# Optimization experiments

Hardware: AMD Instinct MI355X
Metric: run time of the kernel (lower is better)

## Reference

```python
import jax, jax.numpy as jnp
import numpy as np

D_MODEL = 384
D_STATE = 16
D_CONV = 3
EXPAND = 2
D_INNER = EXPAND * D_MODEL          # 768
DT_RANK = (D_MODEL + 15) // 16      # 24 (mamba_ssm 'auto' rank = ceil(d_model/16))
B_, H_, W_ = 8, 32, 32


def setup_inputs() -> dict:
    key = jax.random.key(0)
    ks = jax.random.split(key, 8)
    s = lambda k, shape, scale: jax.random.normal(k, shape, jnp.float32) * scale
    x = jax.random.normal(ks[0], (B_, D_MODEL, H_, W_), jnp.float32)
    in_proj_w = s(ks[1], (2 * D_INNER, D_MODEL), 0.02)
    conv_w = s(ks[2], (D_INNER, D_CONV), 0.1)          # depthwise conv kernels
    conv_b = jnp.zeros((D_INNER,), jnp.float32)
    x_proj_w = s(ks[3], (DT_RANK + 2 * D_STATE, D_INNER), 0.02)
    dt_proj_w = s(ks[4], (D_INNER, DT_RANK), 0.1)
    # bias so that softplus(bias) ~= 0.01 (mamba dt init)
    dt_proj_b = jnp.log(jnp.expm1(jnp.full((D_INNER,), 0.01, jnp.float32)))
    # S4D-real init: A = -[1..N] per channel, stored as log
    A_log = jnp.log(jnp.broadcast_to(
        jnp.arange(1, D_STATE + 1, dtype=jnp.float32), (D_INNER, D_STATE)))
    D = jnp.ones((D_INNER,), jnp.float32)
    out_proj_w = s(ks[5], (D_MODEL, D_INNER), 0.02)
    return dict(x=x, in_proj_w=in_proj_w, conv_w=conv_w, conv_b=conv_b,
                x_proj_w=x_proj_w, dt_proj_w=dt_proj_w, dt_proj_b=dt_proj_b,
                A_log=A_log, D=D, out_proj_w=out_proj_w)


def _mamba(xseq, in_proj_w, conv_w, conv_b, x_proj_w,
           dt_proj_w, dt_proj_b, A_log, D, out_proj_w):
    # xseq: (B, L, d_model)
    B, L, _ = xseq.shape
    xz = xseq @ in_proj_w.T                         # (B, L, 2*d_inner)
    xin, z = jnp.split(xz, 2, axis=-1)

    # depthwise causal conv1d over L
    xc = jnp.transpose(xin, (0, 2, 1))              # (B, d_inner, L)
    xc = jnp.pad(xc, ((0, 0), (0, 0), (D_CONV - 1, 0)))
    xc = jax.lax.conv_general_dilated(
        xc, conv_w[:, None, :], (1,), 'VALID',
        dimension_numbers=('NCH', 'OIH', 'NCH'),
        feature_group_count=D_INNER)
    xc = xc + conv_b[None, :, None]
    u = jax.nn.silu(jnp.transpose(xc, (0, 2, 1)))   # (B, L, d_inner)

    dbc = u @ x_proj_w.T                            # (B, L, dt_rank + 2N)
    dt = dbc[..., :DT_RANK]
    Bm = dbc[..., DT_RANK:DT_RANK + D_STATE]        # (B, L, N)
    Cm = dbc[..., DT_RANK + D_STATE:]               # (B, L, N)
    dt = jax.nn.softplus(dt @ dt_proj_w.T + dt_proj_b)  # (B, L, d_inner)
    A = -jnp.exp(A_log)                             # (d_inner, N)

    def step(h, inp):
        dt_t, B_t, C_t, u_t = inp                   # (B,d), (B,N), (B,N), (B,d)
        dA = jnp.exp(dt_t[..., None] * A)           # (B, d_inner, N)
        h = dA * h + (dt_t * u_t)[..., None] * B_t[:, None, :]
        y = jnp.einsum('bdn,bn->bd', h, C_t)
        return h, y

    h0 = jnp.zeros((B, D_INNER, D_STATE), xseq.dtype)
    _, ys = jax.lax.scan(step, h0, (jnp.swapaxes(dt, 0, 1), jnp.swapaxes(Bm, 0, 1),
                                    jnp.swapaxes(Cm, 0, 1), jnp.swapaxes(u, 0, 1)))
    y = jnp.swapaxes(ys, 0, 1) + u * D              # (B, L, d_inner)
    y = y * jax.nn.silu(z)
    return y @ out_proj_w.T                         # (B, L, d_model)


def reference(x, in_proj_w, conv_w, conv_b, x_proj_w,
              dt_proj_w, dt_proj_b, A_log, D, out_proj_w):
    # x: (B, C, H, W) -> sequence (B, H*W, C) -> Mamba -> back to (B, C, H, W)
    B, C, H, W = x.shape
    xseq = jnp.transpose(x, (0, 2, 3, 1)).reshape(B, H * W, C)
    y = _mamba(xseq, in_proj_w, conv_w, conv_b, x_proj_w,
               dt_proj_w, dt_proj_b, A_log, D, out_proj_w)
    return jnp.transpose(y.reshape(B, H, W, C), (0, 3, 1, 2))
```

## Files before the change

### kernel.cpp

```cpp
#include <hip/hip_runtime.h>

#define D_MODEL 384
#define D_STATE 16
#define D_INNER 768
#define DT_RANK 24
#define NB 8
#define LSEQ 1024
#define NROWS (NB * LSEQ)
#define DBC_N 56
#define SEG 16
#define NSEG 64

typedef unsigned short u16;
typedef __attribute__((ext_vector_type(8))) short bf16x8;
typedef __attribute__((ext_vector_type(4))) float f32x4;

__device__ __forceinline__ float silu(float x) { return x / (1.f + __expf(-x)); }

__device__ __forceinline__ u16 f2bf_rne(float v, float& hval) {
    unsigned u = __builtin_bit_cast(unsigned, v);
    unsigned h = (u + 0x7FFFu + ((u >> 16) & 1u)) >> 16;
    hval = __builtin_bit_cast(float, h << 16);
    return (u16)h;
}

__device__ __forceinline__ void split2(float v, u16& h, u16& l) {
    float hval, dummy;
    h = f2bf_rne(v, hval);
    l = f2bf_rne(v - hval, dummy);
}

template <int CTRL>
__device__ __forceinline__ float dpp_mov(float v) {
    return __builtin_bit_cast(float, __builtin_amdgcn_update_dpp(
        0, __builtin_bit_cast(int, v), CTRL, 0xf, 0xf, false));
}

__global__ __launch_bounds__(256) void k_splits(const float* __restrict__ Wi,
                                                const float* __restrict__ Wo,
                                                const float* __restrict__ Wx,
                                                u16* __restrict__ Wi_hi, u16* __restrict__ Wi_lo,
                                                u16* __restrict__ Wo_hi, u16* __restrict__ Wo_lo,
                                                u16* __restrict__ Wx_hi, u16* __restrict__ Wx_lo) {
    const int NWi = 1536 * 384, NWo = 384 * 768, NWx = 64 * 768;
    const int i = blockIdx.x * 256 + threadIdx.x;
    if (i < NWi) {
        u16 h, l; split2(Wi[i], h, l);
        Wi_hi[i] = h; Wi_lo[i] = l;
    } else if (i < NWi + NWo) {
        const int j = i - NWi;
        u16 h, l; split2(Wo[j], h, l);
        Wo_hi[j] = h; Wo_lo[j] = l;
    } else if (i < NWi + NWo + NWx) {
        const int j = i - NWi - NWo;
        const int row = j / 768;
        u16 h = 0, l = 0;
        if (row < DBC_N) split2(Wx[j], h, l);
        Wx_hi[j] = h; Wx_lo[j] = l;
    }
}

__global__ __launch_bounds__(256) void k_splitT(const float* __restrict__ src,
                                                u16* __restrict__ hi, u16* __restrict__ lo,
                                                int R) {
    __shared__ float s[32][33];
    const int r0 = blockIdx.x * 32, c0 = blockIdx.y * 32, b = blockIdx.z;
    const int t = threadIdx.x;
    const int cc = t & 31, rr = t >> 5;
#pragma unroll
    for (int p = 0; p < 4; ++p)
        s[rr + p * 8][cc] = src[((size_t)b * R + r0 + rr + p * 8) * LSEQ + c0 + cc];
    __syncthreads();
    const int rr2 = t & 31, cc2 = t >> 5;
#pragma unroll
    for (int p = 0; p < 4; ++p) {
        const int c = cc2 + p * 8;
        u16 h, l;
        split2(s[rr2][c], h, l);
        const size_t idx = ((size_t)b * LSEQ + c0 + c) * R + r0 + rr2;
        hi[idx] = h; lo[idx] = l;
    }
}

template <int K>
__global__ __launch_bounds__(256) void k_gemm(const u16* __restrict__ Ahi,
                                              const u16* __restrict__ Alo,
                                              const u16* __restrict__ Bhi,
                                              const u16* __restrict__ Blo,
                                              float* __restrict__ out0,
                                              float* __restrict__ out1) {
    constexpr int KT = K / 32;
    __shared__ u16 lA[2][2][512 * 8];
    __shared__ u16 lB[2][2][512 * 8];
    const int tid = threadIdx.x;
    const int n0 = blockIdx.x * 128;
    const int m0 = blockIdx.y * 128;

    bf16x8 rah[2], ral[2], rbh[2], rbl[2];
    auto load_kt = [&](int kt) {
        const int ko = kt * 32;
#pragma unroll
        for (int i = 0; i < 2; ++i) {
            const int slot = tid + 256 * i;
            const size_t aoff = (size_t)(m0 + (slot & 127)) * K + ko + (slot >> 7) * 8;
            const size_t boff = (size_t)(n0 + (slot & 127)) * K + ko + (slot >> 7) * 8;
            rah[i] = *reinterpret_cast<const bf16x8*>(Ahi + aoff);
            ral[i] = *reinterpret_cast<const bf16x8*>(Alo + aoff);
            rbh[i] = *reinterpret_cast<const bf16x8*>(Bhi + boff);
            rbl[i] = *reinterpret_cast<const bf16x8*>(Blo + boff);
        }
    };
    auto write_kt = [&](int buf) {
#pragma unroll
        for (int i = 0; i < 2; ++i) {
            const int slot = tid + 256 * i;
            *reinterpret_cast<bf16x8*>(&lA[buf][0][slot * 8]) = rah[i];
            *reinterpret_cast<bf16x8*>(&lA[buf][1][slot * 8]) = ral[i];
            *reinterpret_cast<bf16x8*>(&lB[buf][0][slot * 8]) = rbh[i];
            *reinterpret_cast<bf16x8*>(&lB[buf][1][slot * 8]) = rbl[i];
        }
    };

    load_kt(0);
    write_kt(0);
    if (KT > 1) load_kt(1);

    const int lane = tid & 63, w = tid >> 6;
    const int wm = w >> 1, wn = w & 1;
    const int fr = lane & 15, g = lane >> 4;
    const int abase = (g * 128 + wm * 64 + fr) * 8;
    const int bbase = (g * 128 + wn * 64 + fr) * 8;

    f32x4 acc[4][4] = {};
    for (int kt = 0; kt < KT; ++kt) {
        const int cur = kt & 1;
        __syncthreads();
        bf16x8 ah[4], al[4], bh[4], bl[4];
#pragma unroll
        for (int mi = 0; mi < 4; ++mi) {
            ah[mi] = *reinterpret_cast<const bf16x8*>(&lA[cur][0][abase + mi * 128]);
            al[mi] = *reinterpret_cast<const bf16x8*>(&lA[cur][1][abase + mi * 128]);
        }
#pragma unroll
        for (int ni = 0; ni < 4; ++ni) {
            bh[ni] = *reinterpret_cast<const bf16x8*>(&lB[cur][0][bbase + ni * 128]);
            bl[ni] = *reinterpret_cast<const bf16x8*>(&lB[cur][1][bbase + ni * 128]);
        }
#pragma unroll
        for (int mi = 0; mi < 4; ++mi)
#pragma unroll
            for (int ni = 0; ni < 4; ++ni) {
                acc[mi][ni] = __builtin_amdgcn_mfma_f32_16x16x32_bf16(
                    ah[mi], bh[ni], acc[mi][ni], 0, 0, 0);
                acc[mi][ni] = __builtin_amdgcn_mfma_f32_16x16x32_bf16(
                    ah[mi], bl[ni], acc[mi][ni], 0, 0, 0);
                acc[mi][ni] = __builtin_amdgcn_mfma_f32_16x16x32_bf16(
                    al[mi], bh[ni], acc[mi][ni], 0, 0, 0);
            }
        if (kt + 1 < KT) {
            __syncthreads();
            write_kt(cur ^ 1);
            if (kt + 2 < KT) load_kt(kt + 2);
        }
    }

    const int b_idx = m0 >> 10;
    const int l0b = m0 & 1023;
    if (n0 < D_INNER) {
#pragma unroll
        for (int mi = 0; mi < 4; ++mi) {
#pragma unroll
            for (int ni = 0; ni < 4; ++ni) {
                const int m = m0 + wm * 64 + mi * 16 + (lane >> 4) * 4;
                const int n = n0 + wn * 64 + ni * 16 + (lane & 15);
#pragma unroll
                for (int j = 0; j < 4; ++j)
                    out0[(size_t)(m + j) * D_INNER + n] = acc[mi][ni][j];
            }
        }
    } else {
#pragma unroll
        for (int mi = 0; mi < 4; ++mi) {
#pragma unroll
            for (int ni = 0; ni < 4; ++ni) {
                const int l = l0b + wm * 64 + mi * 16 + (lane >> 4) * 4;
                const int d = (n0 - D_INNER) + wn * 64 + ni * 16 + (lane & 15);
                float4 v = make_float4(silu(acc[mi][ni][0]), silu(acc[mi][ni][1]),
                                       silu(acc[mi][ni][2]), silu(acc[mi][ni][3]));
                *reinterpret_cast<float4*>(
                    &out1[((size_t)b_idx * D_INNER + d) * LSEQ + l]) = v;
            }
        }
    }
}

__global__ __launch_bounds__(256) void k_gemmo(const u16* __restrict__ Ahi,
                                               const u16* __restrict__ Alo,
                                               const u16* __restrict__ Bhi,
                                               const u16* __restrict__ Blo,
                                               float* __restrict__ out) {
    constexpr int KT = 24;
    __shared__ u16 lA[2][2][512 * 8];
    __shared__ u16 lB[2][2][256 * 8];
    const int tid = threadIdx.x;
    const int n0 = blockIdx.x * 64;
    const int m0 = blockIdx.y * 128;

    bf16x8 rah[2], ral[2], rbh, rbl;
    auto load_kt = [&](int kt) {
        const int ko = kt * 32;
#pragma unroll
        for (int i = 0; i < 2; ++i) {
            const int slot = tid + 256 * i;
            const size_t aoff = (size_t)(m0 + (slot & 127)) * D_INNER + ko + (slot >> 7) * 8;
            rah[i] = *reinterpret_cast<const bf16x8*>(Ahi + aoff);
            ral[i] = *reinterpret_cast<const bf16x8*>(Alo + aoff);
        }
        const size_t boff = (size_t)(n0 + (tid & 63)) * D_INNER + ko + (tid >> 6) * 8;
        rbh = *reinterpret_cast<const bf16x8*>(Bhi + boff);
        rbl = *reinterpret_cast<const bf16x8*>(Blo + boff);
    };
    auto write_kt = [&](int buf) {
#pragma unroll
        for (int i = 0; i < 2; ++i) {
            const int slot = tid + 256 * i;
            *reinterpret_cast<bf16x8*>(&lA[buf][0][slot * 8]) = rah[i];
            *reinterpret_cast<bf16x8*>(&lA[buf][1][slot * 8]) = ral[i];
        }
        *reinterpret_cast<bf16x8*>(&lB[buf][0][tid * 8]) = rbh;
        *reinterpret_cast<bf16x8*>(&lB[buf][1][tid * 8]) = rbl;
    };

    load_kt(0);
    write_kt(0);
    load_kt(1);

    const int lane = tid & 63, w = tid >> 6;
    const int wm = w >> 1, wn = w & 1;
    const int fr = lane & 15, g = lane >> 4;
    const int abase = (g * 128 + wm * 64 + fr) * 8;
    const int bbase = (g * 64 + wn * 32 + fr) * 8;

    f32x4 acc[4][2] = {};
    for (int kt = 0; kt < KT; ++kt) {
        const int cur = kt & 1;
        __syncthreads();
        bf16x8 ah[4], al[4], bh[2], bl[2];
#pragma unroll
        for (int mi = 0; mi < 4; ++mi) {
            ah[mi] = *reinterpret_cast<const bf16x8*>(&lA[cur][0][abase + mi * 128]);
            al[mi] = *reinterpret_cast<const bf16x8*>(&lA[cur][1][abase + mi * 128]);
        }
#pragma unroll
        for (int ni = 0; ni < 2; ++ni) {
            bh[ni] = *reinterpret_cast<const bf16x8*>(&lB[cur][0][bbase + ni * 128]);
            bl[ni] = *reinterpret_cast<const bf16x8*>(&lB[cur][1][bbase + ni * 128]);
        }
#pragma unroll
        for (int mi = 0; mi < 4; ++mi)
#pragma unroll
            for (int ni = 0; ni < 2; ++ni) {
                acc[mi][ni] = __builtin_amdgcn_mfma_f32_16x16x32_bf16(
                    ah[mi], bh[ni], acc[mi][ni], 0, 0, 0);
                acc[mi][ni] = __builtin_amdgcn_mfma_f32_16x16x32_bf16(
                    ah[mi], bl[ni], acc[mi][ni], 0, 0, 0);
                acc[mi][ni] = __builtin_amdgcn_mfma_f32_16x16x32_bf16(
                    al[mi], bh[ni], acc[mi][ni], 0, 0, 0);
            }
        if (kt + 1 < KT) {
            __syncthreads();
            write_kt(cur ^ 1);
            if (kt + 2 < KT) load_kt(kt + 2);
        }
    }

    const int b_idx = m0 >> 10;
    const int l0b = m0 & 1023;
#pragma unroll
    for (int mi = 0; mi < 4; ++mi) {
#pragma unroll
        for (int ni = 0; ni < 2; ++ni) {
            const int n = n0 + wn * 32 + ni * 16 + fr;
            const int l = l0b + wm * 64 + mi * 16 + g * 4;
            float4 v = make_float4(acc[mi][ni][0], acc[mi][ni][1],
                                   acc[mi][ni][2], acc[mi][ni][3]);
            *reinterpret_cast<float4*>(
                &out[((size_t)b_idx * D_MODEL + n) * LSEQ + l]) = v;
        }
    }
}

__global__ __launch_bounds__(256) void k_xprojm(const u16* __restrict__ Uhi,
                                                const u16* __restrict__ Ulo,
                                                const u16* __restrict__ Whi,
                                                const u16* __restrict__ Wlo,
                                                float* __restrict__ dbc,
                                                float* __restrict__ bct) {
    __shared__ u16 lA[2][2][128 * 8];
    __shared__ u16 lB[2][2][256 * 8];
    const int tid = threadIdx.x;
    const int m0 = blockIdx.x * 32;

    bf16x8 rah, ral, rbh, rbl;
    bool haveA = tid < 128;
    auto load_kt = [&](int kt) {
        const int ko = kt * 32;
        if (haveA) {
            const size_t aoff = (size_t)(m0 + (tid & 31)) * D_INNER + ko + (tid >> 5) * 8;
            rah = *reinterpret_cast<const bf16x8*>(Uhi + aoff);
            ral = *reinterpret_cast<const bf16x8*>(Ulo + aoff);
        }
        const size_t boff = (size_t)(tid & 63) * D_INNER + ko + (tid >> 6) * 8;
        rbh = *reinterpret_cast<const bf16x8*>(Whi + boff);
        rbl = *reinterpret_cast<const bf16x8*>(Wlo + boff);
    };
    auto write_kt = [&](int buf) {
        if (haveA) {
            *reinterpret_cast<bf16x8*>(&lA[buf][0][tid * 8]) = rah;
            *reinterpret_cast<bf16x8*>(&lA[buf][1][tid * 8]) = ral;
        }
        *reinterpret_cast<bf16x8*>(&lB[buf][0][tid * 8]) = rbh;
        *reinterpret_cast<bf16x8*>(&lB[buf][1][tid * 8]) = rbl;
    };

    load_kt(0);
    write_kt(0);
    load_kt(1);

    const int lane = tid & 63, w = tid >> 6;
    const int fr = lane & 15, g = lane >> 4;
    f32x4 acc[2] = {};
    for (int kt = 0; kt < 24; ++kt) {
        const int cur = kt & 1;
        __syncthreads();
        bf16x8 ah[2], al[2];
#pragma unroll
        for (int mi = 0; mi < 2; ++mi) {
            const int af = (g * 32 + mi * 16 + fr) * 8;
            ah[mi] = *reinterpret_cast<const bf16x8*>(&lA[cur][0][af]);
            al[mi] = *reinterpret_cast<const bf16x8*>(&lA[cur][1][af]);
        }
        const int bf = (g * 64 + w * 16 + fr) * 8;
        bf16x8 bh = *reinterpret_cast<const bf16x8*>(&lB[cur][0][bf]);
        bf16x8 bl = *reinterpret_cast<const bf16x8*>(&lB[cur][1][bf]);
#pragma unroll
        for (int mi = 0; mi < 2; ++mi) {
            acc[mi] = __builtin_amdgcn_mfma_f32_16x16x32_bf16(ah[mi], bh, acc[mi], 0, 0, 0);
            acc[mi] = __builtin_amdgcn_mfma_f32_16x16x32_bf16(ah[mi], bl, acc[mi], 0, 0, 0);
            acc[mi] = __builtin_amdgcn_mfma_f32_16x16x32_bf16(al[mi], bh, acc[mi], 0, 0, 0);
        }
        if (kt + 1 < 24) {
            __syncthreads();
            write_kt(cur ^ 1);
            if (kt + 2 < 24) load_kt(kt + 2);
        }
    }

    const int b_idx = m0 >> 10;
    const int col = w * 16 + fr;
#pragma unroll
    for (int mi = 0; mi < 2; ++mi) {
#pragma unroll
        for (int j = 0; j < 4; ++j) {
            const int r = mi * 16 + g * 4 + j;
            const float v = acc[mi][j];
            if (col < DT_RANK) {
                dbc[(size_t)(m0 + r) * DBC_N + col] = v;
            } else if (col < DBC_N) {
                bct[((size_t)b_idx * 32 + (col - DT_RANK)) * LSEQ + ((m0 & 1023) + r)] = v;
            }
        }
    }
}

__global__ __launch_bounds__(256) void k_conv(const float* __restrict__ xin,
                                              const float* __restrict__ cw,
                                              const float* __restrict__ cb,
                                              u16* __restrict__ u_hi,
                                              u16* __restrict__ u_lo,
                                              float* __restrict__ uT) {
    __shared__ float xs[34][32];
    __shared__ float us[32][33];
    const int d0 = blockIdx.x * 32;
    const int l0 = blockIdx.y * 32;
    const int b  = blockIdx.z;
    const int t = threadIdx.x;
    const int dd = t & 31, r = t >> 5;
    for (int rr = r; rr < 34; rr += 8) {
        const int l = l0 - 2 + rr;
        xs[rr][dd] = (l >= 0) ? xin[((size_t)b * LSEQ + l) * D_INNER + d0 + dd] : 0.f;
    }
    __syncthreads();
    const float w0 = cw[(d0 + dd) * 3 + 0], w1 = cw[(d0 + dd) * 3 + 1], w2 = cw[(d0 + dd) * 3 + 2];
    const float bv = cb[d0 + dd];
#pragma unroll
    for (int p = 0; p < 4; ++p) {
        const int li = r + p * 8;
        float acc = bv;
        acc = fmaf(xs[li + 0][dd], w0, acc);
        acc = fmaf(xs[li + 1][dd], w1, acc);
        acc = fmaf(xs[li + 2][dd], w2, acc);
        const float uv = silu(acc);
        u16 h, l;
        split2(uv, h, l);
        const size_t idx = ((size_t)b * LSEQ + l0 + li) * D_INNER + d0 + dd;
        u_hi[idx] = h; u_lo[idx] = l;
        us[li][dd] = uv;
    }
    __syncthreads();
    const int ll = t & 31, dg = t >> 5;
#pragma unroll
    for (int p = 0; p < 4; ++p) {
        const int dl = dg + p * 8;
        uT[((size_t)b * D_INNER + d0 + dl) * LSEQ + l0 + ll] = us[ll][dl];
    }
}

__global__ __launch_bounds__(256) void k_dtproj(const float* __restrict__ dbc,
                                                const float* __restrict__ W,
                                                const float* __restrict__ bias,
                                                float* __restrict__ dtT) {
    __shared__ float sd[64][25];
    __shared__ float sw[64][24];
    __shared__ float sb[64];
    const int d0 = blockIdx.x * 64;
    const int row0 = blockIdx.y * 64;
    const int b = row0 >> 10, lr0 = row0 & 1023;
    const int t = threadIdx.x;
    for (int e = t; e < 64 * 24; e += 256) {
        const int rl = e / 24, rr = e - rl * 24;
        sd[rl][rr] = dbc[(size_t)(row0 + rl) * DBC_N + rr];
        sw[rl][rr] = W[(size_t)(d0 + rl) * DT_RANK + rr];
    }
    if (t < 64) sb[t] = bias[d0 + t];
    __syncthreads();
    const int ll = t & 63, dg = t >> 6;
    for (int dd = 0; dd < 16; ++dd) {
        const int dl = dg * 16 + dd;
        float acc = sb[dl];
#pragma unroll
        for (int r = 0; r < DT_RANK; ++r) acc = fmaf(sd[ll][r], sw[dl][r], acc);
        const float v = (acc > 20.f) ? acc : log1pf(__expf(acc));
        dtT[((size_t)b * D_INNER + d0 + dl) * LSEQ + lr0 + ll] = v;
    }
}

__global__ __launch_bounds__(1024, 8) void k_scan(float* dtyT,
                                                  const float* __restrict__ uT,
                                                  const float* __restrict__ szT,
                                                  const float* __restrict__ bct,
                                                  const float* __restrict__ A_log,
                                                  const float* __restrict__ Dp) {
    __shared__ float dt_s[LSEQ], u_s[LSEQ], sz_s[LSEQ], y_s[LSEQ];
    __shared__ float Pb[16][NSEG + 2], Hb[16][NSEG + 2];
    const int t = threadIdx.x;
    const int d = blockIdx.x;
    const int b = blockIdx.y;
    const size_t base = ((size_t)b * D_INNER + d) * LSEQ;
    if (t < 256) {
        *reinterpret_cast<float4*>(&dt_s[t * 4]) =
            *reinterpret_cast<const float4*>(&dtyT[base + t * 4]);
    } else if (t < 512) {
        const int q = (t - 256) * 4;
        *reinterpret_cast<float4*>(&u_s[q]) = *reinterpret_cast<const float4*>(&uT[base + q]);
    } else if (t < 768) {
        const int q = (t - 512) * 4;
        *reinterpret_cast<float4*>(&sz_s[q]) = *reinterpret_cast<const float4*>(&szT[base + q]);
    }
    const int n = t & 15, seg = t >> 4;
    const float Aval = -__expf(A_log[d * D_STATE + n]);
    const float Dv = Dp[d];
    float Breg[SEG];
    {
        const size_t bb = ((size_t)b * 32 + n) * LSEQ + seg * SEG;
#pragma unroll
        for (int q = 0; q < SEG; q += 4)
            *reinterpret_cast<float4*>(&Breg[q]) = *reinterpret_cast<const float4*>(&bct[bb + q]);
    }
    __syncthreads();
    const int l0 = seg * SEG;
    float h = 0.f, P = 1.f;
#pragma unroll
    for (int l = 0; l < SEG; ++l) {
        const float dtv = dt_s[l0 + l];
        const float a = __expf(dtv * Aval);
        h = fmaf(a, h, dtv * u_s[l0 + l] * Breg[l]);
        P *= a;
    }
    Pb[n][seg] = P;
    Hb[n][seg] = h;
    float Creg[SEG];
    {
        const size_t cc = ((size_t)b * 32 + 16 + n) * LSEQ + seg * SEG;
#pragma unroll
        for (int q = 0; q < SEG; q += 4)
            *reinterpret_cast<float4*>(&Creg[q]) = *reinterpret_cast<const float4*>(&bct[cc + q]);
    }
    __syncthreads();
    {
        const int w = t >> 6, lane = t & 63;
        float Pw = Pb[w][lane], Hw = Hb[w][lane];
#pragma unroll
        for (int off = 1; off < NSEG; off <<= 1) {
            const float Pp = __shfl_up(Pw, off);
            const float Hp = __shfl_up(Hw, off);
            if (lane >= off) {
                Hw = fmaf(Hp, Pw, Hw);
                Pw *= Pp;
            }
        }
        Hb[w][lane] = Hw;
    }
    __syncthreads();
    h = (seg == 0) ? 0.f : Hb[n][seg - 1];
#pragma unroll
    for (int l = 0; l < SEG; ++l) {
        const float dtv = dt_s[l0 + l];
        const float u_v = u_s[l0 + l];
        const float a = __expf(dtv * Aval);
        h = fmaf(a, h, dtv * u_v * Breg[l]);
        float p = h * Creg[l];
        p += dpp_mov<0x128>(p);
        p += dpp_mov<0x124>(p);
        p += dpp_mov<0x122>(p);
        p += dpp_mov<0x121>(p);
        if (n == 0)
            y_s[l0 + l] = fmaf(u_v, Dv, p) * sz_s[l0 + l];
    }
    __syncthreads();
    if (t < 256)
        *reinterpret_cast<float4*>(&dtyT[base + t * 4]) =
            *reinterpret_cast<const float4*>(&y_s[t * 4]);
}

extern "C" void kernel_launch(void* const* d_in, const int* in_sizes, int n_in,
                              void* d_out, int out_size, void* d_ws, size_t ws_size,
                              hipStream_t stream) {
    const float* x         = (const float*)d_in[0];
    const float* in_proj_w = (const float*)d_in[1];
    const float* conv_w    = (const float*)d_in[2];
    const float* conv_b    = (const float*)d_in[3];
    const float* x_proj_w  = (const float*)d_in[4];
    const float* dt_proj_w = (const float*)d_in[5];
    const float* dt_proj_b = (const float*)d_in[6];
    const float* A_log     = (const float*)d_in[7];
    const float* Dp        = (const float*)d_in[8];
    const float* out_proj_w= (const float*)d_in[9];
    float* out = (float*)d_out;

    const size_t SB = (size_t)NROWS * D_INNER * 4;
    char* wsb = (char*)d_ws;
    float* xin   = (float*)(wsb);
    float* szT   = (float*)(wsb + SB);
    u16*  u_hi   = (u16*)  (wsb + 2 * SB);
    u16*  u_lo   = u_hi + (size_t)NROWS * D_INNER;
    float* uT    = (float*)(wsb + 3 * SB);
    float* dbc   = (float*)(wsb + 4 * SB);
    float* bct   = (float*)(wsb + 4 * SB + 1835008);
    u16*  Wi_hi  = (u16*) (wsb + 4 * SB + 1835008 + 1048576);
    u16*  Wi_lo  = Wi_hi + 1536 * 384;
    u16*  Wo_hi  = Wi_lo + 1536 * 384;
    u16*  Wo_lo  = Wo_hi + 384 * 768;
    u16*  Wx_hi  = Wo_lo + 384 * 768;
    u16*  Wx_lo  = Wx_hi + 64 * 768;
    u16*  Ax_hi  = (u16*)uT;
    u16*  Ax_lo  = Ax_hi + (size_t)NROWS * 384;
    u16*  Ay_hi  = (u16*)uT;
    u16*  Ay_lo  = Ay_hi + (size_t)NROWS * 768;
    float* dtyT  = xin;

    const int NSPLIT = 1536 * 384 + 384 * 768 + 64 * 768;
    k_splits<<<(NSPLIT + 255) / 256, 256, 0, stream>>>(in_proj_w, out_proj_w, x_proj_w,
                                                       Wi_hi, Wi_lo, Wo_hi, Wo_lo, Wx_hi, Wx_lo);
    k_splitT<<<dim3(12, 32, NB), 256, 0, stream>>>(x, Ax_hi, Ax_lo, 384);
    k_gemm<384><<<dim3(12, 64), 256, 0, stream>>>(Ax_hi, Ax_lo, Wi_hi, Wi_lo, xin, szT);
    k_conv<<<dim3(24, 32, NB), 256, 0, stream>>>(xin, conv_w, conv_b, u_hi, u_lo, uT);
    k_xprojm<<<NROWS / 32, 256, 0, stream>>>(u_hi, u_lo, Wx_hi, Wx_lo, dbc, bct);
    k_dtproj<<<dim3(12, NROWS / 64), 256, 0, stream>>>(dbc, dt_proj_w, dt_proj_b, dtyT);
    k_scan<<<dim3(D_INNER, NB), 1024, 0, stream>>>(dtyT, uT, szT, bct, A_log, Dp);
    k_splitT<<<dim3(24, 32, NB), 256, 0, stream>>>(dtyT, Ay_hi, Ay_lo, 768);
    k_gemmo<<<dim3(6, 64), 256, 0, stream>>>(Ay_hi, Ay_lo, Wo_hi, Wo_lo, out);
}
```

Before: 293.3 us.

## Use direct global-to-LDS loads in GEMMs and vectorize scan LDS reads

Replaces the register-staged global loads plus LDS writes in the three GEMM kernels with global_load_lds async copies into the alternate LDS buffer, issued at the top of each k-iteration with a single barrier at the end. This aims to cut VGPR pressure and the extra LDS write instructions. The scan kernel now reads dt and u from shared memory as float4, uses exp2f with a prescaled A, and batches the y writes into float4 stores. The risk is that the async LDS loads may not be waited on correctly before the barrier and reads, and the 16-byte global_load_lds form requires gfx950 support.

```diff
diff --git a/kernel.cpp b/kernel.cpp
--- a/kernel.cpp
+++ b/kernel.cpp
@@ -28,6 +28,12 @@
     float hval, dummy;
     h = f2bf_rne(v, hval);
     l = f2bf_rne(v - hval, dummy);
+}
+
+__device__ __forceinline__ void gload16(const u16* g, u16* l) {
+    __builtin_amdgcn_global_load_lds(
+        (const __attribute__((address_space(1))) unsigned int*)g,
+        (__attribute__((address_space(3))) unsigned int*)l, 16, 0, 0);
 }
 
 template <int CTRL>
@@ -96,34 +102,22 @@
     const int n0 = blockIdx.x * 128;
     const int m0 = blockIdx.y * 128;
 
-    bf16x8 rah[2], ral[2], rbh[2], rbl[2];
-    auto load_kt = [&](int kt) {
+    auto stage = [&](int kt, int buf) {
         const int ko = kt * 32;
 #pragma unroll
         for (int i = 0; i < 2; ++i) {
             const int slot = tid + 256 * i;
             const size_t aoff = (size_t)(m0 + (slot & 127)) * K + ko + (slot >> 7) * 8;
             const size_t boff = (size_t)(n0 + (slot & 127)) * K + ko + (slot >> 7) * 8;
-            rah[i] = *reinterpret_cast<const bf16x8*>(Ahi + aoff);
-            ral[i] = *reinterpret_cast<const bf16x8*>(Alo + aoff);
-            rbh[i] = *reinterpret_cast<const bf16x8*>(Bhi + boff);
-            rbl[i] = *reinterpret_cast<const bf16x8*>(Blo + boff);
+            gload16(Ahi + aoff, &lA[buf][0][slot * 8]);
+            gload16(Alo + aoff, &lA[buf][1][slot * 8]);
+            gload16(Bhi + boff, &lB[buf][0][slot * 8]);
+            gload16(Blo + boff, &lB[buf][1][slot * 8]);
         }
     };
-    auto write_kt = [&](int buf) {
-#pragma unroll
-        for (int i = 0; i < 2; ++i) {
-            const int slot = tid + 256 * i;
-            *reinterpret_cast<bf16x8*>(&lA[buf][0][slot * 8]) = rah[i];
-            *reinterpret_cast<bf16x8*>(&lA[buf][1][slot * 8]) = ral[i];
-            *reinterpret_cast<bf16x8*>(&lB[buf][0][slot * 8]) = rbh[i];
-            *reinterpret_cast<bf16x8*>(&lB[buf][1][slot * 8]) = rbl[i];
-        }
-    };
-
-    load_kt(0);
-    write_kt(0);
-    if (KT > 1) load_kt(1);
+
+    stage(0, 0);
+    __syncthreads();
 
     const int lane = tid & 63, w = tid >> 6;
     const int wm = w >> 1, wn = w & 1;
@@ -134,7 +128,7 @@
     f32x4 acc[4][4] = {};
     for (int kt = 0; kt < KT; ++kt) {
         const int cur = kt & 1;
-        __syncthreads();
+        if (kt + 1 < KT) stage(kt + 1, cur ^ 1);
         bf16x8 ah[4], al[4], bh[4], bl[4];
 #pragma unroll
         for (int mi = 0; mi < 4; ++mi) {
@@ -157,11 +151,7 @@
                 acc[mi][ni] = __builtin_amdgcn_mfma_f32_16x16x32_bf16(
                     al[mi], bh[ni], acc[mi][ni], 0, 0, 0);
             }
-        if (kt + 1 < KT) {
-            __syncthreads();
-            write_kt(cur ^ 1);
-            if (kt + 2 < KT) load_kt(kt + 2);
-        }
+        __syncthreads();
     }
 
     const int b_idx = m0 >> 10;
@@ -171,11 +161,11 @@
         for (int mi = 0; mi < 4; ++mi) {
 #pragma unroll
             for (int ni = 0; ni < 4; ++ni) {
-                const int m = m0 + wm * 64 + mi * 16 + (lane >> 4) * 4;
-                const int n = n0 + wn * 64 + ni * 16 + (lane & 15);
+                const int m = m0 + wm * 64 + mi * 16 + g * 4;
+                const int nn = n0 + wn * 64 + ni * 16 + fr;
 #pragma unroll
                 for (int j = 0; j < 4; ++j)
-                    out0[(size_t)(m + j) * D_INNER + n] = acc[mi][ni][j];
+                    out0[(size_t)(m + j) * D_INNER + nn] = acc[mi][ni][j];
             }
         }
     } else {
@@ -183,12 +173,12 @@
         for (int mi = 0; mi < 4; ++mi) {
 #pragma unroll
             for (int ni = 0; ni < 4; ++ni) {
-                const int l = l0b + wm * 64 + mi * 16 + (lane >> 4) * 4;
-                const int d = (n0 - D_INNER) + wn * 64 + ni * 16 + (lane & 15);
+                const int l = l0b + wm * 64 + mi * 16 + g * 4;
+                const int dd = (n0 - D_INNER) + wn * 64 + ni * 16 + fr;
                 float4 v = make_float4(silu(acc[mi][ni][0]), silu(acc[mi][ni][1]),
                                        silu(acc[mi][ni][2]), silu(acc[mi][ni][3]));
                 *reinterpret_cast<float4*>(
-                    &out1[((size_t)b_idx * D_INNER + d) * LSEQ + l]) = v;
+                    &out1[((size_t)b_idx * D_INNER + dd) * LSEQ + l]) = v;
             }
         }
     }
@@ -206,34 +196,22 @@
     const int n0 = blockIdx.x * 64;
     const int m0 = blockIdx.y * 128;
 
-    bf16x8 rah[2], ral[2], rbh, rbl;
-    auto load_kt = [&](int kt) {
+    auto stage = [&](int kt, int buf) {
         const int ko = kt * 32;
 #pragma unroll
         for (int i = 0; i < 2; ++i) {
             const int slot = tid + 256 * i;
             const size_t aoff = (size_t)(m0 + (slot & 127)) * D_INNER + ko + (slot >> 7) * 8;
-            rah[i] = *reinterpret_cast<const bf16x8*>(Ahi + aoff);
-            ral[i] = *reinterpret_cast<const bf16x8*>(Alo + aoff);
+            gload16(Ahi + aoff, &lA[buf][0][slot * 8]);
+            gload16(Alo + aoff, &lA[buf][1][slot * 8]);
         }
         const size_t boff = (size_t)(n0 + (tid & 63)) * D_INNER + ko + (tid >> 6) * 8;
-        rbh = *reinterpret_cast<const bf16x8*>(Bhi + boff);
-        rbl = *reinterpret_cast<const bf16x8*>(Blo + boff);
+        gload16(Bhi + boff, &lB[buf][0][tid * 8]);
+        gload16(Blo + boff, &lB[buf][1][tid * 8]);
     };
-    auto write_kt = [&](int buf) {
-#pragma unroll
-        for (int i = 0; i < 2; ++i) {
-            const int slot = tid + 256 * i;
-            *reinterpret_cast<bf16x8*>(&lA[buf][0][slot * 8]) = rah[i];
-            *reinterpret_cast<bf16x8*>(&lA[buf][1][slot * 8]) = ral[i];
-        }
-        *reinterpret_cast<bf16x8*>(&lB[buf][0][tid * 8]) = rbh;
-        *reinterpret_cast<bf16x8*>(&lB[buf][1][tid * 8]) = rbl;
-    };
-
-    load_kt(0);
-    write_kt(0);
-    load_kt(1);
+
+    stage(0, 0);
+    __syncthreads();
 
     const int lane = tid & 63, w = tid >> 6;
     const int wm = w >> 1, wn = w & 1;
@@ -244,7 +222,7 @@
     f32x4 acc[4][2] = {};
     for (int kt = 0; kt < KT; ++kt) {
         const int cur = kt & 1;
-        __syncthreads();
+        if (kt + 1 < KT) stage(kt + 1, cur ^ 1);
         bf16x8 ah[4], al[4], bh[2], bl[2];
 #pragma unroll
         for (int mi = 0; mi < 4; ++mi) {
@@ -267,11 +245,7 @@
                 acc[mi][ni] = __builtin_amdgcn_mfma_f32_16x16x32_bf16(
                     al[mi], bh[ni], acc[mi][ni], 0, 0, 0);
             }
-        if (kt + 1 < KT) {
-            __syncthreads();
-            write_kt(cur ^ 1);
-            if (kt + 2 < KT) load_kt(kt + 2);
-        }
+        __syncthreads();
     }
 
     const int b_idx = m0 >> 10;
@@ -280,12 +254,12 @@
     for (int mi = 0; mi < 4; ++mi) {
 #pragma unroll
         for (int ni = 0; ni < 2; ++ni) {
-            const int n = n0 + wn * 32 + ni * 16 + fr;
+            const int nn = n0 + wn * 32 + ni * 16 + fr;
             const int l = l0b + wm * 64 + mi * 16 + g * 4;
             float4 v = make_float4(acc[mi][ni][0], acc[mi][ni][1],
                                    acc[mi][ni][2], acc[mi][ni][3]);
             *reinterpret_cast<float4*>(
-                &out[((size_t)b_idx * D_MODEL + n) * LSEQ + l]) = v;
+                &out[((size_t)b_idx * D_MODEL + nn) * LSEQ + l]) = v;
         }
     }
 }
@@ -301,38 +275,27 @@
     const int tid = threadIdx.x;
     const int m0 = blockIdx.x * 32;
 
-    bf16x8 rah, ral, rbh, rbl;
-    bool haveA = tid < 128;
-    auto load_kt = [&](int kt) {
+    auto stage = [&](int kt, int buf) {
         const int ko = kt * 32;
-        if (haveA) {
+        if (tid < 128) {
             const size_t aoff = (size_t)(m0 + (tid & 31)) * D_INNER + ko + (tid >> 5) * 8;
-            rah = *reinterpret_cast<const bf16x8*>(Uhi + aoff);
-            ral = *reinterpret_cast<const bf16x8*>(Ulo + aoff);
+            gload16(Uhi + aoff, &lA[buf][0][tid * 8]);
+            gload16(Ulo + aoff, &lA[buf][1][tid * 8]);
         }
         const size_t boff = (size_t)(tid & 63) * D_INNER + ko + (tid >> 6) * 8;
-        rbh = *reinterpret_cast<const bf16x8*>(Whi + boff);
-        rbl = *reinterpret_cast<const bf16x8*>(Wlo + boff);
+        gload16(Whi + boff, &lB[buf][0][tid * 8]);
+        gload16(Wlo + boff, &lB[buf][1][tid * 8]);
     };
-    auto write_kt = [&](int buf) {
-        if (haveA) {
-            *reinterpret_cast<bf16x8*>(&lA[buf][0][tid * 8]) = rah;
-            *reinterpret_cast<bf16x8*>(&lA[buf][1][tid * 8]) = ral;
-        }
-        *reinterpret_cast<bf16x8*>(&lB[buf][0][tid * 8]) = rbh;
-        *reinterpret_cast<bf16x8*>(&lB[buf][1][tid * 8]) = rbl;
-    };
-
-    load_kt(0);
-    write_kt(0);
-    load_kt(1);
+
+    stage(0, 0);
+    __syncthreads();
 
     const int lane = tid & 63, w = tid >> 6;
     const int fr = lane & 15, g = lane >> 4;
     f32x4 acc[2] = {};
     for (int kt = 0; kt < 24; ++kt) {
         const int cur = kt & 1;
-        __syncthreads();
+        if (kt + 1 < 24) stage(kt + 1, cur ^ 1);
         bf16x8 ah[2], al[2];
 #pragma unroll
         for (int mi = 0; mi < 2; ++mi) {
@@ -349,11 +312,7 @@
             acc[mi] = __builtin_amdgcn_mfma_f32_16x16x32_bf16(ah[mi], bl, acc[mi], 0, 0, 0);
             acc[mi] = __builtin_amdgcn_mfma_f32_16x16x32_bf16(al[mi], bh, acc[mi], 0, 0, 0);
         }
-        if (kt + 1 < 24) {
-            __syncthreads();
-            write_kt(cur ^ 1);
-            if (kt + 2 < 24) load_kt(kt + 2);
-        }
+        __syncthreads();
     }
 
     const int b_idx = m0 >> 10;
@@ -468,7 +427,7 @@
         *reinterpret_cast<float4*>(&sz_s[q]) = *reinterpret_cast<const float4*>(&szT[base + q]);
     }
     const int n = t & 15, seg = t >> 4;
-    const float Aval = -__expf(A_log[d * D_STATE + n]);
+    const float Aval2 = -__expf(A_log[d * D_STATE + n]) * 1.44269504088896f;
     const float Dv = Dp[d];
     float Breg[SEG];
     {
@@ -481,11 +440,14 @@
     const int l0 = seg * SEG;
     float h = 0.f, P = 1.f;
 #pragma unroll
-    for (int l = 0; l < SEG; ++l) {
-        const float dtv = dt_s[l0 + l];
-        const float a = __expf(dtv * Aval);
-        h = fmaf(a, h, dtv * u_s[l0 + l] * Breg[l]);
-        P *= a;
+    for (int j = 0; j < 4; ++j) {
+        const float4 dt4 = *reinterpret_cast<const float4*>(&dt_s[l0 + j * 4]);
+        const float4 u4  = *reinterpret_cast<const float4*>(&u_s[l0 + j * 4]);
+        float a;
+        a = exp2f(dt4.x * Aval2); h = fmaf(a, h, dt4.x * u4.x * Breg[j * 4 + 0]); P *= a;
+        a = exp2f(dt4.y * Aval2); h = fmaf(a, h, dt4.y * u4.y * Breg[j * 4 + 1]); P *= a;
+        a = exp2f(dt4.z * Aval2); h = fmaf(a, h, dt4.z * u4.z * Breg[j * 4 + 2]); P *= a;
+        a = exp2f(dt4.w * Aval2); h = fmaf(a, h, dt4.w * u4.w * Breg[j * 4 + 3]); P *= a;
     }
     Pb[n][seg] = P;
     Hb[n][seg] = h;
@@ -514,18 +476,39 @@
     __syncthreads();
     h = (seg == 0) ? 0.f : Hb[n][seg - 1];
 #pragma unroll
-    for (int l = 0; l < SEG; ++l) {
-        const float dtv = dt_s[l0 + l];
-        const float u_v = u_s[l0 + l];
-        const float a = __expf(dtv * Aval);
-        h = fmaf(a, h, dtv * u_v * Breg[l]);
-        float p = h * Creg[l];
-        p += dpp_mov<0x128>(p);
-        p += dpp_mov<0x124>(p);
-        p += dpp_mov<0x122>(p);
-        p += dpp_mov<0x121>(p);
-        if (n == 0)
-            y_s[l0 + l] = fmaf(u_v, Dv, p) * sz_s[l0 + l];
+    for (int j = 0; j < 4; ++j) {
+        const float4 dt4 = *reinterpret_cast<const float4*>(&dt_s[l0 + j * 4]);
+        const float4 u4  = *reinterpret_cast<const float4*>(&u_s[l0 + j * 4]);
+        float a, p, y0, y1, y2, y3;
+        a = exp2f(dt4.x * Aval2); h = fmaf(a, h, dt4.x * u4.x * Breg[j * 4 + 0]);
+        p = h * Creg[j * 4 + 0];
+        p += dpp_mov<0x128>(p); p += dpp_mov<0x124>(p);
+        p += dpp_mov<0x122>(p); p += dpp_mov<0x121>(p);
+        y0 = p;
+        a = exp2f(dt4.y * Aval2); h = fmaf(a, h, dt4.y * u4.y * Breg[j * 4 + 1]);
+        p = h * Creg[j * 4 + 1];
+        p += dpp_mov<0x128>(p); p += dpp_mov<0x124>(p);
+        p += dpp_mov<0x122>(p); p += dpp_mov<0x121>(p);
+        y1 = p;
+        a = exp2f(dt4.z * Aval2); h = fmaf(a, h, dt4.z * u4.z * Breg[j * 4 + 2]);
+        p = h * Creg[j * 4 + 2];
+        p += dpp_mov<0x128>(p); p += dpp_mov<0x124>(p);
+        p += dpp_mov<0x122>(p); p += dpp_mov<0x121>(p);
+        y2 = p;
+        a = exp2f(dt4.w * Aval2); h = fmaf(a, h, dt4.w * u4.w * Breg[j * 4 + 3]);
+        p = h * Creg[j * 4 + 3];
+        p += dpp_mov<0x128>(p); p += dpp_mov<0x124>(p);
+        p += dpp_mov<0x122>(p); p += dpp_mov<0x121>(p);
+        y3 = p;
+        if (n == 0) {
+            const float4 sz4 = *reinterpret_cast<const float4*>(&sz_s[l0 + j * 4]);
+            float4 yy;
+            yy.x = fmaf(u4.x, Dv, y0) * sz4.x;
+            yy.y = fmaf(u4.y, Dv, y1) * sz4.y;
+            yy.z = fmaf(u4.z, Dv, y2) * sz4.z;
+            yy.w = fmaf(u4.w, Dv, y3) * sz4.w;
+            *reinterpret_cast<float4*>(&y_s[l0 + j * 4]) = yy;
+        }
     }
     __syncthreads();
     if (t < 256)
```

Result: slower. 327.2 us (+11.5%).
